# Performance work log

Hardware: AMD Instinct MI355X
Metric: run time of the kernel (lower is better)

Reference implementation:

```python
import jax, jax.numpy as jnp
import numpy as np

D = 3            # sde dimension
M_I = 20         # gaussians per axis -> m = M_I**D = 8000
K = 16384        # batch of positions
SIGMA_I = 1.0    # scalar covariance diagonal
NORMALIZED = True


def _grid_means():
    # uniform grid over domain [-3, 3]^D, matching np.mgrid with m_i points per axis
    axes = [np.linspace(-3.0, 3.0, M_I) for _ in range(D)]
    g = np.stack(np.meshgrid(*axes, indexing='ij'), axis=-1).reshape(-1, D)
    return jnp.asarray(g, dtype=jnp.float32)


def setup_inputs() -> dict:
    key = jax.random.key(0)
    kx, kt = jax.random.split(key)
    x = jax.random.normal(kx, (K, D), dtype=jnp.float32)
    means = _grid_means()                      # (m, d)
    theta = jax.random.normal(kt, (means.shape[0],), dtype=jnp.float32)
    return {"x": x, "means": means, "theta": theta}


def reference(x, means, theta):
    # x: (K, d), means: (m, d), theta: (m,)
    sigma = jnp.float32(SIGMA_I)
    diff = x[:, None, :] - means[None, :, :]                  # (K, m, d)
    log_basis = -0.5 * jnp.sum(diff * diff, axis=2) / sigma   # (K, m)
    if NORMALIZED:
        log_basis = log_basis - jnp.float32(np.log(2.0 * np.pi * SIGMA_I) * D / 2.0)
    basis = jnp.exp(log_basis)                                # (K, m)
    # grad basis = -(diff / sigma) * basis[..., None]; weighted sum over m
    out = -jnp.einsum('kmd,km,m->kd', diff, basis, theta) / sigma
    return out
```

## Files before the change

kernel.cpp:

```cpp
#include <hip/hip_runtime.h>


#define NG   20
#define MTOT 8000
#define KPB  256
#define IC   2
#define NCHUNK (NG / IC)

__global__ __launch_bounds__(KPB) void gauss_factored_kernel(
    const float* __restrict__ x, const float* __restrict__ means,
    const float* __restrict__ theta, float* __restrict__ out) {
  __shared__ float sth[MTOT];
  __shared__ float sg[3 * NG];

  const int tid = threadIdx.x;

  {
    const float4* th4 = (const float4*)theta;
    float4* sth4 = (float4*)sth;
    for (int idx = tid; idx < MTOT / 4; idx += KPB) sth4[idx] = th4[idx];
  }
  if (tid < 3 * NG) {
    int axis = tid / NG, p = tid % NG;
    int m = (axis == 0) ? p * 400 : (axis == 1) ? p * 20 : p;
    sg[tid] = means[m * 3 + axis];
  }
  __syncthreads();

  const int k = blockIdx.x * KPB + tid;
  const float x0 = x[k * 3 + 0];
  const float x1 = x[k * 3 + 1];
  const float x2 = x[k * 3 + 2];

  float Ey[NG], Eyp[NG], Ez[NG], Ezp[NG];
#pragma unroll
  for (int j = 0; j < NG; ++j) {
    float dy = x1 - sg[NG + j];
    float e = __expf(-0.5f * dy * dy);
    Ey[j] = e;
    Eyp[j] = -dy * e;
  }
#pragma unroll
  for (int l = 0; l < NG; ++l) {
    float dz = x2 - sg[2 * NG + l];
    float e = __expf(-0.5f * dz * dz);
    Ez[l] = e;
    Ezp[l] = -dz * e;
  }

  float o0 = 0.f, o1 = 0.f, o2 = 0.f;
  const int i0 = blockIdx.y * IC;

#pragma unroll
  for (int ii = 0; ii < IC; ++ii) {
    const int i = i0 + ii;
    const float dxv = x0 - sg[i];
    const float ex = __expf(-0.5f * dxv * dxv);
    const float exn = -dxv * ex;

    float b = 0.f, b1 = 0.f, b2 = 0.f;
    const float* thrown = &sth[i * 400];
#pragma unroll
    for (int j = 0; j < NG; ++j) {
      const float4* trow = (const float4*)(thrown + j * NG);
      float aZ0 = 0.f, aZ1 = 0.f, aZp0 = 0.f, aZp1 = 0.f;
#pragma unroll
      for (int l4 = 0; l4 < 5; ++l4) {
        const float4 t = trow[l4];
        aZ0  = fmaf(t.x, Ez [4 * l4 + 0], aZ0);
        aZp0 = fmaf(t.x, Ezp[4 * l4 + 0], aZp0);
        aZ1  = fmaf(t.y, Ez [4 * l4 + 1], aZ1);
        aZp1 = fmaf(t.y, Ezp[4 * l4 + 1], aZp1);
        aZ0  = fmaf(t.z, Ez [4 * l4 + 2], aZ0);
        aZp0 = fmaf(t.z, Ezp[4 * l4 + 2], aZp0);
        aZ1  = fmaf(t.w, Ez [4 * l4 + 3], aZ1);
        aZp1 = fmaf(t.w, Ezp[4 * l4 + 3], aZp1);
      }
      const float aZ = aZ0 + aZ1;
      const float aZp = aZp0 + aZp1;
      b  = fmaf(Ey[j],  aZ,  b);
      b1 = fmaf(Eyp[j], aZ,  b1);
      b2 = fmaf(Ey[j],  aZp, b2);
    }
    o0 = fmaf(exn, b, o0);
    o1 = fmaf(ex, b1, o1);
    o2 = fmaf(ex, b2, o2);
  }

  const float Nc = 0.06349363593424097f;
  atomicAdd(&out[k * 3 + 0], o0 * Nc);
  atomicAdd(&out[k * 3 + 1], o1 * Nc);
  atomicAdd(&out[k * 3 + 2], o2 * Nc);
}

extern "C" void kernel_launch(void* const* d_in, const int* in_sizes, int n_in,
                              void* d_out, int out_size, void* d_ws, size_t ws_size,
                              hipStream_t stream) {
  const float* x = (const float*)d_in[0];
  const float* means = (const float*)d_in[1];
  const float* theta = (const float*)d_in[2];
  float* out = (float*)d_out;

  const int K = in_sizes[0] / 3;

  hipMemsetAsync(out, 0, (size_t)out_size * sizeof(float), stream);

  dim3 grid(K / KPB, NCHUNK);
  gauss_factored_kernel<<<grid, KPB, 0, stream>>>(x, means, theta, out);
}
```

Before: 70.07 us.

## Split i-chunks across warps in-block and reduce via shared memory instead of atomics

Each block now handles 64 positions with 4 wavefronts, each covering 5 x-axis slices, and combines the partial sums through shared memory. This replaces the 2D grid of 640 blocks plus global atomics and the memset with 256 blocks that write the output directly. Y-axis exponentials are computed on the fly inside the j loop and reused across the 5 slices, which lowers register use. The theta load into shared memory is amortised over more work per block, but there are fewer blocks overall and an extra block barrier.

```diff
diff --git a/kernel.cpp b/kernel.cpp
--- a/kernel.cpp
+++ b/kernel.cpp
@@ -3,22 +3,24 @@
 
 #define NG   20
 #define MTOT 8000
-#define KPB  256
-#define IC   2
-#define NCHUNK (NG / IC)
+#define KB   64
+#define NCH  4
+#define IC   (NG / NCH)
+#define NT   (KB * NCH)
 
-__global__ __launch_bounds__(KPB) void gauss_factored_kernel(
+__global__ __launch_bounds__(NT) void gauss_factored_kernel(
     const float* __restrict__ x, const float* __restrict__ means,
     const float* __restrict__ theta, float* __restrict__ out) {
   __shared__ float sth[MTOT];
   __shared__ float sg[3 * NG];
+  __shared__ float sred[NCH * KB * 3];
 
   const int tid = threadIdx.x;
 
   {
     const float4* th4 = (const float4*)theta;
     float4* sth4 = (float4*)sth;
-    for (int idx = tid; idx < MTOT / 4; idx += KPB) sth4[idx] = th4[idx];
+    for (int idx = tid; idx < MTOT / 4; idx += NT) sth4[idx] = th4[idx];
   }
   if (tid < 3 * NG) {
     int axis = tid / NG, p = tid % NG;
@@ -27,19 +29,14 @@
   }
   __syncthreads();
 
-  const int k = blockIdx.x * KPB + tid;
+  const int klocal = tid & (KB - 1);
+  const int chunk = tid >> 6;
+  const int k = blockIdx.x * KB + klocal;
   const float x0 = x[k * 3 + 0];
   const float x1 = x[k * 3 + 1];
   const float x2 = x[k * 3 + 2];
 
-  float Ey[NG], Eyp[NG], Ez[NG], Ezp[NG];
-#pragma unroll
-  for (int j = 0; j < NG; ++j) {
-    float dy = x1 - sg[NG + j];
-    float e = __expf(-0.5f * dy * dy);
-    Ey[j] = e;
-    Eyp[j] = -dy * e;
-  }
+  float Ez[NG], Ezp[NG];
 #pragma unroll
   for (int l = 0; l < NG; ++l) {
     float dz = x2 - sg[2 * NG + l];
@@ -48,21 +45,28 @@
     Ezp[l] = -dz * e;
   }
 
-  float o0 = 0.f, o1 = 0.f, o2 = 0.f;
-  const int i0 = blockIdx.y * IC;
-
+  const int i0 = chunk * IC;
+  float ex[IC], exn[IC];
 #pragma unroll
   for (int ii = 0; ii < IC; ++ii) {
-    const int i = i0 + ii;
-    const float dxv = x0 - sg[i];
-    const float ex = __expf(-0.5f * dxv * dxv);
-    const float exn = -dxv * ex;
+    float dx = x0 - sg[i0 + ii];
+    float e = __expf(-0.5f * dx * dx);
+    ex[ii] = e;
+    exn[ii] = -dx * e;
+  }
 
-    float b = 0.f, b1 = 0.f, b2 = 0.f;
-    const float* thrown = &sth[i * 400];
+  float b[IC], b1[IC], b2[IC];
 #pragma unroll
-    for (int j = 0; j < NG; ++j) {
-      const float4* trow = (const float4*)(thrown + j * NG);
+  for (int ii = 0; ii < IC; ++ii) { b[ii] = 0.f; b1[ii] = 0.f; b2[ii] = 0.f; }
+
+#pragma unroll 4
+  for (int j = 0; j < NG; ++j) {
+    const float dy = x1 - sg[NG + j];
+    const float Ey = __expf(-0.5f * dy * dy);
+    const float Eyp = -dy * Ey;
+#pragma unroll
+    for (int ii = 0; ii < IC; ++ii) {
+      const float4* trow = (const float4*)&sth[(i0 + ii) * 400 + j * NG];
       float aZ0 = 0.f, aZ1 = 0.f, aZp0 = 0.f, aZp1 = 0.f;
 #pragma unroll
       for (int l4 = 0; l4 < 5; ++l4) {
@@ -78,19 +82,30 @@
       }
       const float aZ = aZ0 + aZ1;
       const float aZp = aZp0 + aZp1;
-      b  = fmaf(Ey[j],  aZ,  b);
-      b1 = fmaf(Eyp[j], aZ,  b1);
-      b2 = fmaf(Ey[j],  aZp, b2);
+      b[ii]  = fmaf(Ey,  aZ,  b[ii]);
+      b1[ii] = fmaf(Eyp, aZ,  b1[ii]);
+      b2[ii] = fmaf(Ey,  aZp, b2[ii]);
     }
-    o0 = fmaf(exn, b, o0);
-    o1 = fmaf(ex, b1, o1);
-    o2 = fmaf(ex, b2, o2);
   }
 
-  const float Nc = 0.06349363593424097f;
-  atomicAdd(&out[k * 3 + 0], o0 * Nc);
-  atomicAdd(&out[k * 3 + 1], o1 * Nc);
-  atomicAdd(&out[k * 3 + 2], o2 * Nc);
+  float o0 = 0.f, o1 = 0.f, o2 = 0.f;
+#pragma unroll
+  for (int ii = 0; ii < IC; ++ii) {
+    o0 = fmaf(exn[ii], b[ii], o0);
+    o1 = fmaf(ex[ii], b1[ii], o1);
+    o2 = fmaf(ex[ii], b2[ii], o2);
+  }
+
+  sred[chunk * (KB * 3) + klocal * 3 + 0] = o0;
+  sred[chunk * (KB * 3) + klocal * 3 + 1] = o1;
+  sred[chunk * (KB * 3) + klocal * 3 + 2] = o2;
+  __syncthreads();
+
+  if (tid < KB * 3) {
+    const float Nc = 0.06349363593424097f;
+    float s = sred[tid] + sred[KB * 3 + tid] + sred[2 * KB * 3 + tid] + sred[3 * KB * 3 + tid];
+    out[blockIdx.x * (KB * 3) + tid] = s * Nc;
+  }
 }
 
 extern "C" void kernel_launch(void* const* d_in, const int* in_sizes, int n_in,
@@ -103,8 +118,5 @@
 
   const int K = in_sizes[0] / 3;
 
-  hipMemsetAsync(out, 0, (size_t)out_size * sizeof(float), stream);
-
-  dim3 grid(K / KPB, NCHUNK);
-  gauss_factored_kernel<<<grid, KPB, 0, stream>>>(x, means, theta, out);
+  gauss_factored_kernel<<<dim3(K / KB), NT, 0, stream>>>(x, means, theta, out);
 }
```

Measured after the change: 72.60 us. 3.6% more time.

## Restructure work split: two positions per thread, one x-slice per wavefront, deterministic reduction

Applied to the files above, without the earlier changes.

Each thread now handles two positions and each wavefront handles one x-grid index, so every shared-memory theta load feeds twice as many FMAs. The y-axis exponentials are computed inside the loop instead of being stored in register arrays. The memset and global atomics are replaced by an in-block shared-memory reduction across the four wavefronts, a workspace write, and a second kernel that sums the five x-chunks and applies the normalisation. This adds a second launch and workspace traffic, and raises register pressure from the four per-position z arrays.

```diff
diff --git a/kernel.cpp b/kernel.cpp
--- a/kernel.cpp
+++ b/kernel.cpp
@@ -1,24 +1,27 @@
 #include <hip/hip_runtime.h>
 
 
-#define NG   20
-#define MTOT 8000
-#define KPB  256
-#define IC   2
-#define NCHUNK (NG / IC)
+#define NG    20
+#define MTOT  8000
+#define NT    256
+#define KPT   2
+#define KPB   128
+#define IPB   4
+#define NCG   5
 
-__global__ __launch_bounds__(KPB) void gauss_factored_kernel(
+__global__ __launch_bounds__(NT) void gauss_main(
     const float* __restrict__ x, const float* __restrict__ means,
-    const float* __restrict__ theta, float* __restrict__ out) {
+    const float* __restrict__ theta, float* __restrict__ ws, int K) {
   __shared__ float sth[MTOT];
   __shared__ float sg[3 * NG];
+  __shared__ float sred[IPB][KPB * 3];
 
   const int tid = threadIdx.x;
 
   {
     const float4* th4 = (const float4*)theta;
-    float4* sth4 = (float4*)sth;
-    for (int idx = tid; idx < MTOT / 4; idx += KPB) sth4[idx] = th4[idx];
+    float4* s4 = (float4*)sth;
+    for (int idx = tid; idx < MTOT / 4; idx += NT) s4[idx] = th4[idx];
   }
   if (tid < 3 * NG) {
     int axis = tid / NG, p = tid % NG;
@@ -27,70 +30,107 @@
   }
   __syncthreads();
 
-  const int k = blockIdx.x * KPB + tid;
-  const float x0 = x[k * 3 + 0];
-  const float x1 = x[k * 3 + 1];
-  const float x2 = x[k * 3 + 2];
+  const int lane = tid & 63;
+  const int wv = tid >> 6;
+  const int i = blockIdx.y * IPB + wv;
+  const int k0 = blockIdx.x * KPB + lane;
+  const int k1 = k0 + 64;
 
-  float Ey[NG], Eyp[NG], Ez[NG], Ezp[NG];
-#pragma unroll
-  for (int j = 0; j < NG; ++j) {
-    float dy = x1 - sg[NG + j];
-    float e = __expf(-0.5f * dy * dy);
-    Ey[j] = e;
-    Eyp[j] = -dy * e;
-  }
+  const float x00 = x[k0 * 3 + 0], x01 = x[k0 * 3 + 1], x02 = x[k0 * 3 + 2];
+  const float x10 = x[k1 * 3 + 0], x11 = x[k1 * 3 + 1], x12 = x[k1 * 3 + 2];
+
+  float Ez0[NG], Ezp0[NG], Ez1[NG], Ezp1[NG];
 #pragma unroll
   for (int l = 0; l < NG; ++l) {
-    float dz = x2 - sg[2 * NG + l];
-    float e = __expf(-0.5f * dz * dz);
-    Ez[l] = e;
-    Ezp[l] = -dz * e;
+    const float g = sg[2 * NG + l];
+    const float dz0 = x02 - g;
+    const float e0 = __expf(-0.5f * dz0 * dz0);
+    Ez0[l] = e0; Ezp0[l] = -dz0 * e0;
+    const float dz1 = x12 - g;
+    const float e1 = __expf(-0.5f * dz1 * dz1);
+    Ez1[l] = e1; Ezp1[l] = -dz1 * e1;
   }
 
-  float o0 = 0.f, o1 = 0.f, o2 = 0.f;
-  const int i0 = blockIdx.y * IC;
+  const float gi = sg[i];
+  const float dx0 = x00 - gi, dx1 = x10 - gi;
+  const float ex0 = __expf(-0.5f * dx0 * dx0), ex1 = __expf(-0.5f * dx1 * dx1);
+  const float exn0 = -dx0 * ex0, exn1 = -dx1 * ex1;
 
+  float A0 = 0.f, A1 = 0.f, A2 = 0.f;
+  float B0 = 0.f, B1 = 0.f, B2 = 0.f;
+  const float4* trow = (const float4*)&sth[i * 400];
+
+#pragma unroll 2
+  for (int j = 0; j < NG; ++j) {
+    const float gj = sg[NG + j];
+    const float dy0 = x01 - gj, dy1 = x11 - gj;
+    const float Ey0 = __expf(-0.5f * dy0 * dy0);
+    const float Ey1 = __expf(-0.5f * dy1 * dy1);
+    const float Eyp0 = -dy0 * Ey0, Eyp1 = -dy1 * Ey1;
+
+    float z0 = 0.f, zp0 = 0.f, z1 = 0.f, zp1 = 0.f;
+    float y0 = 0.f, yp0 = 0.f, y1 = 0.f, yp1 = 0.f;
 #pragma unroll
-  for (int ii = 0; ii < IC; ++ii) {
-    const int i = i0 + ii;
-    const float dxv = x0 - sg[i];
-    const float ex = __expf(-0.5f * dxv * dxv);
-    const float exn = -dxv * ex;
-
-    float b = 0.f, b1 = 0.f, b2 = 0.f;
-    const float* thrown = &sth[i * 400];
-#pragma unroll
-    for (int j = 0; j < NG; ++j) {
-      const float4* trow = (const float4*)(thrown + j * NG);
-      float aZ0 = 0.f, aZ1 = 0.f, aZp0 = 0.f, aZp1 = 0.f;
-#pragma unroll
-      for (int l4 = 0; l4 < 5; ++l4) {
-        const float4 t = trow[l4];
-        aZ0  = fmaf(t.x, Ez [4 * l4 + 0], aZ0);
-        aZp0 = fmaf(t.x, Ezp[4 * l4 + 0], aZp0);
-        aZ1  = fmaf(t.y, Ez [4 * l4 + 1], aZ1);
-        aZp1 = fmaf(t.y, Ezp[4 * l4 + 1], aZp1);
-        aZ0  = fmaf(t.z, Ez [4 * l4 + 2], aZ0);
-        aZp0 = fmaf(t.z, Ezp[4 * l4 + 2], aZp0);
-        aZ1  = fmaf(t.w, Ez [4 * l4 + 3], aZ1);
-        aZp1 = fmaf(t.w, Ezp[4 * l4 + 3], aZp1);
-      }
-      const float aZ = aZ0 + aZ1;
-      const float aZp = aZp0 + aZp1;
-      b  = fmaf(Ey[j],  aZ,  b);
-      b1 = fmaf(Eyp[j], aZ,  b1);
-      b2 = fmaf(Ey[j],  aZp, b2);
+    for (int l4 = 0; l4 < 5; ++l4) {
+      const float4 t = trow[j * 5 + l4];
+      z0  = fmaf(t.x, Ez0 [4 * l4 + 0], z0);
+      zp0 = fmaf(t.x, Ezp0[4 * l4 + 0], zp0);
+      z1  = fmaf(t.x, Ez1 [4 * l4 + 0], z1);
+      zp1 = fmaf(t.x, Ezp1[4 * l4 + 0], zp1);
+      y0  = fmaf(t.y, Ez0 [4 * l4 + 1], y0);
+      yp0 = fmaf(t.y, Ezp0[4 * l4 + 1], yp0);
+      y1  = fmaf(t.y, Ez1 [4 * l4 + 1], y1);
+      yp1 = fmaf(t.y, Ezp1[4 * l4 + 1], yp1);
+      z0  = fmaf(t.z, Ez0 [4 * l4 + 2], z0);
+      zp0 = fmaf(t.z, Ezp0[4 * l4 + 2], zp0);
+      z1  = fmaf(t.z, Ez1 [4 * l4 + 2], z1);
+      zp1 = fmaf(t.z, Ezp1[4 * l4 + 2], zp1);
+      y0  = fmaf(t.w, Ez0 [4 * l4 + 3], y0);
+      yp0 = fmaf(t.w, Ezp0[4 * l4 + 3], yp0);
+      y1  = fmaf(t.w, Ez1 [4 * l4 + 3], y1);
+      yp1 = fmaf(t.w, Ezp1[4 * l4 + 3], yp1);
     }
-    o0 = fmaf(exn, b, o0);
-    o1 = fmaf(ex, b1, o1);
-    o2 = fmaf(ex, b2, o2);
+    const float aZ0 = z0 + y0, aZp0 = zp0 + yp0;
+    const float aZ1 = z1 + y1, aZp1 = zp1 + yp1;
+    A0 = fmaf(Ey0,  aZ0,  A0);
+    A1 = fmaf(Eyp0, aZ0,  A1);
+    A2 = fmaf(Ey0,  aZp0, A2);
+    B0 = fmaf(Ey1,  aZ1,  B0);
+    B1 = fmaf(Eyp1, aZ1,  B1);
+    B2 = fmaf(Ey1,  aZp1, B2);
   }
 
+  sred[wv][lane * 3 + 0] = exn0 * A0;
+  sred[wv][lane * 3 + 1] = ex0 * A1;
+  sred[wv][lane * 3 + 2] = ex0 * A2;
+  sred[wv][192 + lane * 3 + 0] = exn1 * B0;
+  sred[wv][192 + lane * 3 + 1] = ex1 * B1;
+  sred[wv][192 + lane * 3 + 2] = ex1 * B2;
+  __syncthreads();
+
+  float* wdst = ws + (size_t)blockIdx.y * (size_t)(K * 3) + (size_t)blockIdx.x * (KPB * 3);
+  for (int idx = tid; idx < KPB * 3; idx += NT) {
+    wdst[idx] = sred[0][idx] + sred[1][idx] + sred[2][idx] + sred[3][idx];
+  }
+}
+
+__global__ __launch_bounds__(256) void gauss_reduce(
+    const float* __restrict__ ws, float* __restrict__ out, int n4) {
+  const int idx = blockIdx.x * 256 + threadIdx.x;
+  if (idx >= n4) return;
+  const float4* w4 = (const float4*)ws;
+  const float4 a = w4[idx];
+  const float4 b = w4[n4 + idx];
+  const float4 c = w4[2 * n4 + idx];
+  const float4 d = w4[3 * n4 + idx];
+  const float4 e = w4[4 * n4 + idx];
   const float Nc = 0.06349363593424097f;
-  atomicAdd(&out[k * 3 + 0], o0 * Nc);
-  atomicAdd(&out[k * 3 + 1], o1 * Nc);
-  atomicAdd(&out[k * 3 + 2], o2 * Nc);
+  float4 r;
+  r.x = (a.x + b.x + c.x + d.x + e.x) * Nc;
+  r.y = (a.y + b.y + c.y + d.y + e.y) * Nc;
+  r.z = (a.z + b.z + c.z + d.z + e.z) * Nc;
+  r.w = (a.w + b.w + c.w + d.w + e.w) * Nc;
+  ((float4*)out)[idx] = r;
 }
 
 extern "C" void kernel_launch(void* const* d_in, const int* in_sizes, int n_in,
@@ -100,11 +140,12 @@
   const float* means = (const float*)d_in[1];
   const float* theta = (const float*)d_in[2];
   float* out = (float*)d_out;
+  float* ws = (float*)d_ws;
 
   const int K = in_sizes[0] / 3;
 
-  hipMemsetAsync(out, 0, (size_t)out_size * sizeof(float), stream);
+  gauss_main<<<dim3(K / KPB, NCG), NT, 0, stream>>>(x, means, theta, ws, K);
 
-  dim3 grid(K / KPB, NCHUNK);
-  gauss_factored_kernel<<<grid, KPB, 0, stream>>>(x, means, theta, out);
+  const int n4 = (K * 3) / 4;
+  gauss_reduce<<<dim3((n4 + 255) / 256), 256, 0, stream>>>(ws, out, n4);
 }
```

Measured after the change: 70.62 us. No clear change (+0.8%).
